# Kernel tuning notes

Measured on AMD Instinct MI355X. Metric: run time of the kernel, lower is better.

The kernel has to match this reference:

```python
import jax, jax.numpy as jnp
import numpy as np

INPUT_SIZE = 512
HIDDEN_SIZE = 512
BATCH = 16384


def _layer_norm(x, gamma, beta, eps=1e-5):
    mean = jnp.mean(x, axis=-1, keepdims=True)
    var = jnp.var(x, axis=-1, keepdims=True)
    return (x - mean) * jax.lax.rsqrt(var + eps) * gamma + beta


def setup_inputs() -> dict:
    key = jax.random.key(0)
    ks = jax.random.split(key, 4)
    H = HIDDEN_SIZE
    x = jax.random.normal(ks[0], (BATCH, INPUT_SIZE), dtype=jnp.float32)
    h = jax.random.normal(ks[1], (BATCH, H), dtype=jnp.float32)
    # Linear weights stored torch-style as [out_features, in_features]
    W_i2h = jax.random.normal(ks[2], (3 * H, INPUT_SIZE), dtype=jnp.float32) / np.sqrt(INPUT_SIZE)
    W_h2h = jax.random.normal(ks[3], (3 * H, H), dtype=jnp.float32) / np.sqrt(H)
    return {
        "x": x,
        "h": h,
        "W_i2h": W_i2h,
        "W_h2h": W_h2h,
        "g_r": jnp.ones((H,), jnp.float32), "b_r": jnp.zeros((H,), jnp.float32),
        "g_z": jnp.ones((H,), jnp.float32), "b_z": jnp.zeros((H,), jnp.float32),
        "g_n": jnp.ones((H,), jnp.float32), "b_n": jnp.zeros((H,), jnp.float32),
    }


def reference(x, h, W_i2h, W_h2h, g_r, b_r, g_z, b_z, g_n, b_n):
    H = h.shape[-1]
    x_gates = x @ W_i2h.T  # [B, 3H]
    h_gates = h @ W_h2h.T  # [B, 3H]
    x_r, x_z, x_n = jnp.split(x_gates, 3, axis=1)
    h_r, h_z, h_n = jnp.split(h_gates, 3, axis=1)
    r = jax.nn.sigmoid(_layer_norm(x_r + h_r, g_r, b_r))
    z = jax.nn.sigmoid(_layer_norm(x_z + h_z, g_z, b_z))
    n = jnp.tanh(_layer_norm(x_n + r * h_n, g_n, b_n))
    h_new = (1.0 - z) * n + z * h
    return h_new
```

## Files before the change

### kernel.cpp

```cpp
#include <hip/hip_runtime.h>

#define BATCH 16384
#define BM    64
#define NT    1024

typedef float f32x4 __attribute__((ext_vector_type(4)));
typedef short s16x8 __attribute__((ext_vector_type(8)));

__device__ __forceinline__ unsigned short f2bf(float f) {
  unsigned u = __float_as_uint(f);
  u = (u + 0x7fffu + ((u >> 16) & 1u)) >> 16;
  return (unsigned short)u;
}
__device__ __forceinline__ float bflo(unsigned p) { return __uint_as_float(p << 16); }
__device__ __forceinline__ float bfhi(unsigned p) { return __uint_as_float(p & 0xffff0000u); }

__global__ __launch_bounds__(256) void wconv_kernel(
    const float* __restrict__ wx, const float* __restrict__ wh,
    unsigned short* __restrict__ dst) {
  int i = blockIdx.x * 256 + threadIdx.x;
  const float4* src = (i < 196608) ? (const float4*)wx
                                   : ((const float4*)wh) - 196608;
  float4 v = src[i];
  ushort4 p = {f2bf(v.x), f2bf(v.y), f2bf(v.z), f2bf(v.w)};
  ((ushort4*)dst)[i] = p;
}

__global__ __launch_bounds__(NT, 4) void gru_fused_kernel(
    const float* __restrict__ x, const float* __restrict__ h,
    const unsigned short* __restrict__ Wxb, const unsigned short* __restrict__ Whb,
    const float* __restrict__ g_r, const float* __restrict__ b_r,
    const float* __restrict__ g_z, const float* __restrict__ b_z,
    const float* __restrict__ g_n, const float* __restrict__ b_n,
    float* __restrict__ out) {
  __shared__ __align__(16) unsigned short At[2][BM * 512];
  __shared__ float red[BM][33];
  __shared__ float rstat[BM][2];

  const int tid  = threadIdx.x;
  const int lane = tid & 63;
  const int w    = tid >> 6;
  const int l15  = lane & 15;
  const int lg   = lane >> 4;
  const int rowbase = blockIdx.x * BM;
  const int c0 = w * 32 + l15, c1 = c0 + 16;

  {
    const float4* x4 = (const float4*)x;
    const float4* h4 = (const float4*)h;
    const int sr = tid >> 7, sc4 = tid & 127;
#pragma unroll
    for (int p = 0; p < 8; ++p) {
      int r = p * 8 + sr;
      float4 vx = x4[(size_t)(rowbase + r) * 128 + sc4];
      float4 vh = h4[(size_t)(rowbase + r) * 128 + sc4];
      int bo = (r * 1024 + sc4 * 8) ^ ((r & 7) << 4);
      ushort4 px = {f2bf(vx.x), f2bf(vx.y), f2bf(vx.z), f2bf(vx.w)};
      ushort4 ph = {f2bf(vh.x), f2bf(vh.y), f2bf(vh.z), f2bf(vh.w)};
      *(ushort4*)((char*)At[0] + bo) = px;
      *(ushort4*)((char*)At[1] + bo) = ph;
    }
  }
  __syncthreads();

  f32x4 acc[4][2];

#define ZERO_ACC                                                               \
  _Pragma("unroll")                                                            \
  for (int rf = 0; rf < 4; ++rf)                                               \
    _Pragma("unroll")                                                          \
    for (int cf = 0; cf < 2; ++cf) acc[rf][cf] = (f32x4){0.f, 0.f, 0.f, 0.f};

#define KLOOP(ATP, WPTR, GBASE)                                                \
  {                                                                            \
    const char* wbase = (const char*)(WPTR);                                   \
    _Pragma("unroll 2")                                                        \
    for (int kk = 0; kk < 16; ++kk) {                                          \
      s16x8 af[4];                                                             \
      _Pragma("unroll")                                                        \
      for (int rf = 0; rf < 4; ++rf) {                                         \
        int row = rf * 16 + l15;                                               \
        int bo = (row * 1024 + kk * 64 + lg * 16) ^ ((row & 7) << 4);          \
        af[rf] = *(const s16x8*)((const char*)(ATP) + bo);                     \
      }                                                                        \
      s16x8 bf[2];                                                             \
      _Pragma("unroll")                                                        \
      for (int cf = 0; cf < 2; ++cf) {                                         \
        int wrow = (GBASE) + w * 32 + cf * 16 + l15;                           \
        bf[cf] = *(const s16x8*)(wbase + ((size_t)wrow * 512 + lg * 8) * 2 + kk * 64); \
      }                                                                        \
      _Pragma("unroll")                                                        \
      for (int rf = 0; rf < 4; ++rf)                                           \
        _Pragma("unroll")                                                      \
        for (int cf = 0; cf < 2; ++cf)                                         \
          acc[rf][cf] = __builtin_amdgcn_mfma_f32_16x16x32_bf16(af[rf], bf[cf], acc[rf][cf], 0, 0, 0); \
    }                                                                          \
  }

#define REDUCE_STATS                                                           \
  {                                                                            \
    _Pragma("unroll")                                                          \
    for (int rf = 0; rf < 4; ++rf) {                                           \
      _Pragma("unroll")                                                        \
      for (int rg = 0; rg < 4; ++rg) {                                         \
        float v0 = acc[rf][0][rg], v1 = acc[rf][1][rg];                        \
        float s = v0 + v1, q = v0 * v0 + v1 * v1;                              \
        s += __shfl_xor(s, 1); q += __shfl_xor(q, 1);                          \
        s += __shfl_xor(s, 2); q += __shfl_xor(q, 2);                          \
        s += __shfl_xor(s, 4); q += __shfl_xor(q, 4);                          \
        s += __shfl_xor(s, 8); q += __shfl_xor(q, 8);                          \
        if (l15 == 0) {                                                        \
          red[rf * 16 + lg * 4 + rg][w * 2]     = s;                           \
          red[rf * 16 + lg * 4 + rg][w * 2 + 1] = q;                           \
        }                                                                      \
      }                                                                        \
    }                                                                          \
    __syncthreads();                                                           \
    if (tid < 64) {                                                            \
      float s = 0.f, q = 0.f;                                                  \
      _Pragma("unroll")                                                        \
      for (int ww = 0; ww < 16; ++ww) {                                        \
        s += red[tid][ww * 2];                                                 \
        q += red[tid][ww * 2 + 1];                                             \
      }                                                                        \
      float mean = s * (1.0f / 512.0f);                                        \
      float var  = q * (1.0f / 512.0f) - mean * mean;                          \
      rstat[tid][0] = mean;                                                    \
      rstat[tid][1] = rsqrtf(var + 1e-5f);                                     \
    }                                                                          \
    __syncthreads();                                                           \
  }

  ZERO_ACC
  KLOOP(At[0], Wxb, 0)
  KLOOP(At[1], Whb, 0)
  REDUCE_STATS

  unsigned rp[4][2][2];
  {
    float ga[2] = {g_r[c0], g_r[c1]}, be[2] = {b_r[c0], b_r[c1]};
#pragma unroll
    for (int rf = 0; rf < 4; ++rf)
#pragma unroll
      for (int rg = 0; rg < 4; rg += 2) {
        int row0 = rf * 16 + lg * 4 + rg;
        float m0 = rstat[row0][0], s0 = rstat[row0][1];
        float m1 = rstat[row0 + 1][0], s1 = rstat[row0 + 1][1];
#pragma unroll
        for (int cf = 0; cf < 2; ++cf) {
          float r0 = (acc[rf][cf][rg] - m0) * s0 * ga[cf] + be[cf];
          float r1 = (acc[rf][cf][rg + 1] - m1) * s1 * ga[cf] + be[cf];
          r0 = 1.0f / (1.0f + __expf(-r0));
          r1 = 1.0f / (1.0f + __expf(-r1));
          rp[rf][cf][rg >> 1] = (unsigned)f2bf(r0) | ((unsigned)f2bf(r1) << 16);
        }
      }
  }

  ZERO_ACC
  KLOOP(At[1], Whb, 1024)
#pragma unroll
  for (int rf = 0; rf < 4; ++rf)
#pragma unroll
    for (int cf = 0; cf < 2; ++cf) {
      acc[rf][cf][0] *= bflo(rp[rf][cf][0]);
      acc[rf][cf][1] *= bfhi(rp[rf][cf][0]);
      acc[rf][cf][2] *= bflo(rp[rf][cf][1]);
      acc[rf][cf][3] *= bfhi(rp[rf][cf][1]);
    }
  KLOOP(At[0], Wxb, 1024)
  REDUCE_STATS

  f32x4 nv[4][2];
  {
    float ga[2] = {g_n[c0], g_n[c1]}, be[2] = {b_n[c0], b_n[c1]};
#pragma unroll
    for (int rf = 0; rf < 4; ++rf)
#pragma unroll
      for (int rg = 0; rg < 4; ++rg) {
        int row = rf * 16 + lg * 4 + rg;
        float m = rstat[row][0], sd = rstat[row][1];
#pragma unroll
        for (int cf = 0; cf < 2; ++cf) {
          float arg = (acc[rf][cf][rg] - m) * sd * ga[cf] + be[cf];
          arg = fminf(fmaxf(arg, -20.f), 20.f);
          float e = __expf(2.0f * arg);
          nv[rf][cf][rg] = (e - 1.0f) / (e + 1.0f);
        }
      }
  }

  ZERO_ACC
  KLOOP(At[0], Wxb, 512)
  KLOOP(At[1], Whb, 512)
  REDUCE_STATS

  {
    float ga[2] = {g_z[c0], g_z[c1]}, be[2] = {b_z[c0], b_z[c1]};
#pragma unroll
    for (int rf = 0; rf < 4; ++rf)
#pragma unroll
      for (int rg = 0; rg < 4; ++rg) {
        int row = rf * 16 + lg * 4 + rg;
        float m = rstat[row][0], sd = rstat[row][1];
        int grow = rowbase + row;
#pragma unroll
        for (int cf = 0; cf < 2; ++cf) {
          float zv = (acc[rf][cf][rg] - m) * sd * ga[cf] + be[cf];
          zv = 1.0f / (1.0f + __expf(-zv));
          int gcol = w * 32 + cf * 16 + l15;
          float hval = h[(size_t)grow * 512 + gcol];
          float n = nv[rf][cf][rg];
          out[(size_t)grow * 512 + gcol] = n + zv * (hval - n);
        }
      }
  }
}

extern "C" void kernel_launch(void* const* d_in, const int* in_sizes, int n_in,
                              void* d_out, int out_size, void* d_ws, size_t ws_size,
                              hipStream_t stream) {
  const float* x  = (const float*)d_in[0];
  const float* h  = (const float*)d_in[1];
  const float* wx = (const float*)d_in[2];
  const float* wh = (const float*)d_in[3];
  const float* g_r = (const float*)d_in[4];
  const float* b_r = (const float*)d_in[5];
  const float* g_z = (const float*)d_in[6];
  const float* b_z = (const float*)d_in[7];
  const float* g_n = (const float*)d_in[8];
  const float* b_n = (const float*)d_in[9];
  float* out = (float*)d_out;

  unsigned short* wbf = (unsigned short*)d_ws;

  wconv_kernel<<<1536, 256, 0, stream>>>(wx, wh, wbf);
  gru_fused_kernel<<<BATCH / BM, NT, 0, stream>>>(
      x, h, wbf, wbf + 1536 * 512, g_r, b_r, g_z, b_z, g_n, b_n, out);
}
```

Baseline: 233.6 us.

## Split batch across a 512-thread register-pipelined kernel and the original kernel

Adds a new 512-thread kernel where each wave computes 64 columns with 4x4 accumulator fragments and double-buffered A/B register prefetch across the K loop. It handles the first 160 row blocks, and the original 1024-thread kernel handles the remaining 96 blocks, launched as a second kernel with a row offset. The aim is more MFMA work per loaded fragment and better hiding of weight-load latency, plus an uneven split that fits one wave of blocks on the CUs. The cost is higher register pressure (waves_per_eu 2) and a second serialized launch on the same stream, which may leave tail imbalance.

```diff
diff --git a/kernel.cpp b/kernel.cpp
--- a/kernel.cpp
+++ b/kernel.cpp
@@ -2,7 +2,9 @@
 
 #define BATCH 16384
 #define BM    64
-#define NT    1024
+#define NT    512
+#define NA_BLOCKS 160
+#define NB_BLOCKS 96
 
 typedef float f32x4 __attribute__((ext_vector_type(4)));
 typedef short s16x8 __attribute__((ext_vector_type(8)));
@@ -26,7 +28,9 @@
   ((ushort4*)dst)[i] = p;
 }
 
-__global__ __launch_bounds__(NT, 4) void gru_fused_kernel(
+__global__
+__attribute__((amdgpu_flat_work_group_size(NT, NT), amdgpu_waves_per_eu(2, 2)))
+void gru_pipe_kernel(
     const float* __restrict__ x, const float* __restrict__ h,
     const unsigned short* __restrict__ Wxb, const unsigned short* __restrict__ Whb,
     const float* __restrict__ g_r, const float* __restrict__ b_r,
@@ -34,7 +38,7 @@
     const float* __restrict__ g_n, const float* __restrict__ b_n,
     float* __restrict__ out) {
   __shared__ __align__(16) unsigned short At[2][BM * 512];
-  __shared__ float red[BM][33];
+  __shared__ float red[BM][17];
   __shared__ float rstat[BM][2];
 
   const int tid  = threadIdx.x;
@@ -43,6 +47,218 @@
   const int l15  = lane & 15;
   const int lg   = lane >> 4;
   const int rowbase = blockIdx.x * BM;
+  const int cb = w * 64 + l15;
+
+  {
+    const float4* x4 = (const float4*)x;
+    const float4* h4 = (const float4*)h;
+    const int sr = tid >> 7, sc4 = tid & 127;
+#pragma unroll
+    for (int p = 0; p < 16; ++p) {
+      int r = p * 4 + sr;
+      float4 vx = x4[(size_t)(rowbase + r) * 128 + sc4];
+      float4 vh = h4[(size_t)(rowbase + r) * 128 + sc4];
+      int bo = (r * 1024 + sc4 * 8) ^ ((r & 7) << 4);
+      ushort4 px = {f2bf(vx.x), f2bf(vx.y), f2bf(vx.z), f2bf(vx.w)};
+      ushort4 ph = {f2bf(vh.x), f2bf(vh.y), f2bf(vh.z), f2bf(vh.w)};
+      *(ushort4*)((char*)At[0] + bo) = px;
+      *(ushort4*)((char*)At[1] + bo) = ph;
+    }
+  }
+  __syncthreads();
+
+  f32x4 acc[4][4];
+
+#define ZERO_ACC                                                               \
+  _Pragma("unroll")                                                            \
+  for (int rf = 0; rf < 4; ++rf)                                               \
+    _Pragma("unroll")                                                          \
+    for (int cf = 0; cf < 4; ++cf) acc[rf][cf] = (f32x4){0.f, 0.f, 0.f, 0.f};
+
+#define LOADA(DST, ATP, KK)                                                    \
+  {                                                                            \
+    _Pragma("unroll")                                                          \
+    for (int rf = 0; rf < 4; ++rf) {                                           \
+      int row = rf * 16 + l15;                                                 \
+      int bo = (row * 1024 + (KK) * 64 + lg * 16) ^ ((row & 7) << 4);          \
+      (DST)[rf] = *(const s16x8*)((const char*)(ATP) + bo);                    \
+    }                                                                          \
+  }
+
+#define KLOOP(ATP, WPTR, GBASE)                                                \
+  {                                                                            \
+    const char* wbp[4];                                                        \
+    _Pragma("unroll")                                                          \
+    for (int cf = 0; cf < 4; ++cf)                                             \
+      wbp[cf] = (const char*)(WPTR) +                                          \
+          ((size_t)((GBASE) + w * 64 + cf * 16 + l15) * 512 + lg * 8) * 2;     \
+    s16x8 af[2][4];                                                            \
+    s16x8 bq[2][4];                                                            \
+    LOADA(af[0], ATP, 0)                                                       \
+    _Pragma("unroll")                                                          \
+    for (int cf = 0; cf < 4; ++cf) bq[0][cf] = *(const s16x8*)(wbp[cf]);       \
+    _Pragma("unroll")                                                          \
+    for (int kk = 0; kk < 16; ++kk) {                                          \
+      if (kk < 15) {                                                           \
+        LOADA(af[(kk + 1) & 1], ATP, kk + 1)                                   \
+        _Pragma("unroll")                                                      \
+        for (int cf = 0; cf < 4; ++cf)                                         \
+          bq[(kk + 1) & 1][cf] = *(const s16x8*)(wbp[cf] + (kk + 1) * 64);     \
+      }                                                                        \
+      _Pragma("unroll")                                                        \
+      for (int rf = 0; rf < 4; ++rf)                                           \
+        _Pragma("unroll")                                                      \
+        for (int cf = 0; cf < 4; ++cf)                                         \
+          acc[rf][cf] = __builtin_amdgcn_mfma_f32_16x16x32_bf16(               \
+              af[kk & 1][rf], bq[kk & 1][cf], acc[rf][cf], 0, 0, 0);           \
+    }                                                                          \
+  }
+
+#define REDUCE_STATS                                                           \
+  {                                                                            \
+    _Pragma("unroll")                                                          \
+    for (int rf = 0; rf < 4; ++rf) {                                           \
+      _Pragma("unroll")                                                        \
+      for (int rg = 0; rg < 4; ++rg) {                                         \
+        float v0 = acc[rf][0][rg], v1 = acc[rf][1][rg];                        \
+        float v2 = acc[rf][2][rg], v3 = acc[rf][3][rg];                        \
+        float s = (v0 + v1) + (v2 + v3);                                       \
+        float q = (v0 * v0 + v1 * v1) + (v2 * v2 + v3 * v3);                   \
+        s += __shfl_xor(s, 1); q += __shfl_xor(q, 1);                          \
+        s += __shfl_xor(s, 2); q += __shfl_xor(q, 2);                          \
+        s += __shfl_xor(s, 4); q += __shfl_xor(q, 4);                          \
+        s += __shfl_xor(s, 8); q += __shfl_xor(q, 8);                          \
+        if (l15 == 0) {                                                        \
+          red[rf * 16 + lg * 4 + rg][w * 2]     = s;                           \
+          red[rf * 16 + lg * 4 + rg][w * 2 + 1] = q;                           \
+        }                                                                      \
+      }                                                                        \
+    }                                                                          \
+    __syncthreads();                                                           \
+    if (tid < 64) {                                                            \
+      float s = 0.f, q = 0.f;                                                  \
+      _Pragma("unroll")                                                        \
+      for (int ww = 0; ww < 8; ++ww) {                                         \
+        s += red[tid][ww * 2];                                                 \
+        q += red[tid][ww * 2 + 1];                                             \
+      }                                                                        \
+      float mean = s * (1.0f / 512.0f);                                        \
+      float var  = q * (1.0f / 512.0f) - mean * mean;                          \
+      rstat[tid][0] = mean;                                                    \
+      rstat[tid][1] = rsqrtf(var + 1e-5f);                                     \
+    }                                                                          \
+    __syncthreads();                                                           \
+  }
+
+  ZERO_ACC
+  KLOOP(At[0], Wxb, 0)
+  KLOOP(At[1], Whb, 0)
+  REDUCE_STATS
+
+  unsigned rp[4][4][2];
+  {
+    float ga[4], be[4];
+#pragma unroll
+    for (int cf = 0; cf < 4; ++cf) { ga[cf] = g_r[cb + cf * 16]; be[cf] = b_r[cb + cf * 16]; }
+#pragma unroll
+    for (int rf = 0; rf < 4; ++rf)
+#pragma unroll
+      for (int rg = 0; rg < 4; rg += 2) {
+        int row0 = rf * 16 + lg * 4 + rg;
+        float m0 = rstat[row0][0], s0 = rstat[row0][1];
+        float m1 = rstat[row0 + 1][0], s1 = rstat[row0 + 1][1];
+#pragma unroll
+        for (int cf = 0; cf < 4; ++cf) {
+          float r0 = (acc[rf][cf][rg] - m0) * s0 * ga[cf] + be[cf];
+          float r1 = (acc[rf][cf][rg + 1] - m1) * s1 * ga[cf] + be[cf];
+          r0 = 1.0f / (1.0f + __expf(-r0));
+          r1 = 1.0f / (1.0f + __expf(-r1));
+          rp[rf][cf][rg >> 1] = (unsigned)f2bf(r0) | ((unsigned)f2bf(r1) << 16);
+        }
+      }
+  }
+
+  ZERO_ACC
+  KLOOP(At[1], Whb, 1024)
+#pragma unroll
+  for (int rf = 0; rf < 4; ++rf)
+#pragma unroll
+    for (int cf = 0; cf < 4; ++cf) {
+      acc[rf][cf][0] *= bflo(rp[rf][cf][0]);
+      acc[rf][cf][1] *= bfhi(rp[rf][cf][0]);
+      acc[rf][cf][2] *= bflo(rp[rf][cf][1]);
+      acc[rf][cf][3] *= bfhi(rp[rf][cf][1]);
+    }
+  KLOOP(At[0], Wxb, 1024)
+  REDUCE_STATS
+
+  f32x4 nv[4][4];
+  {
+    float ga[4], be[4];
+#pragma unroll
+    for (int cf = 0; cf < 4; ++cf) { ga[cf] = g_n[cb + cf * 16]; be[cf] = b_n[cb + cf * 16]; }
+#pragma unroll
+    for (int rf = 0; rf < 4; ++rf)
+#pragma unroll
+      for (int rg = 0; rg < 4; ++rg) {
+        int row = rf * 16 + lg * 4 + rg;
+        float m = rstat[row][0], sd = rstat[row][1];
+#pragma unroll
+        for (int cf = 0; cf < 4; ++cf) {
+          float arg = (acc[rf][cf][rg] - m) * sd * ga[cf] + be[cf];
+          arg = fminf(fmaxf(arg, -20.f), 20.f);
+          float e = __expf(2.0f * arg);
+          nv[rf][cf][rg] = (e - 1.0f) / (e + 1.0f);
+        }
+      }
+  }
+
+  ZERO_ACC
+  KLOOP(At[0], Wxb, 512)
+  KLOOP(At[1], Whb, 512)
+  REDUCE_STATS
+
+  {
+    float ga[4], be[4];
+#pragma unroll
+    for (int cf = 0; cf < 4; ++cf) { ga[cf] = g_z[cb + cf * 16]; be[cf] = b_z[cb + cf * 16]; }
+#pragma unroll
+    for (int rf = 0; rf < 4; ++rf)
+#pragma unroll
+      for (int rg = 0; rg < 4; ++rg) {
+        int row = rf * 16 + lg * 4 + rg;
+        float m = rstat[row][0], sd = rstat[row][1];
+        int grow = rowbase + row;
+#pragma unroll
+        for (int cf = 0; cf < 4; ++cf) {
+          float zv = (acc[rf][cf][rg] - m) * sd * ga[cf] + be[cf];
+          zv = 1.0f / (1.0f + __expf(-zv));
+          int gcol = w * 64 + cf * 16 + l15;
+          float hval = h[(size_t)grow * 512 + gcol];
+          float n = nv[rf][cf][rg];
+          out[(size_t)grow * 512 + gcol] = n + zv * (hval - n);
+        }
+      }
+  }
+}
+
+__global__ __launch_bounds__(1024, 4) void gru_base_kernel(
+    const float* __restrict__ x, const float* __restrict__ h,
+    const unsigned short* __restrict__ Wxb, const unsigned short* __restrict__ Whb,
+    const float* __restrict__ g_r, const float* __restrict__ b_r,
+    const float* __restrict__ g_z, const float* __restrict__ b_z,
+    const float* __restrict__ g_n, const float* __restrict__ b_n,
+    float* __restrict__ out, int rowoff) {
+  __shared__ __align__(16) unsigned short At[2][BM * 512];
+  __shared__ float red[BM][33];
+  __shared__ float rstat[BM][2];
+
+  const int tid  = threadIdx.x;
+  const int lane = tid & 63;
+  const int w    = tid >> 6;
+  const int l15  = lane & 15;
+  const int lg   = lane >> 4;
+  const int rowbase = rowoff + blockIdx.x * BM;
   const int c0 = w * 32 + l15, c1 = c0 + 16;
 
   {
@@ -65,13 +281,13 @@
 
   f32x4 acc[4][2];
 
-#define ZERO_ACC                                                               \
+#define ZERO_ACC_B                                                             \
   _Pragma("unroll")                                                            \
   for (int rf = 0; rf < 4; ++rf)                                               \
     _Pragma("unroll")                                                          \
     for (int cf = 0; cf < 2; ++cf) acc[rf][cf] = (f32x4){0.f, 0.f, 0.f, 0.f};
 
-#define KLOOP(ATP, WPTR, GBASE)                                                \
+#define KLOOP_B(ATP, WPTR, GBASE)                                              \
   {                                                                            \
     const char* wbase = (const char*)(WPTR);                                   \
     _Pragma("unroll 2")                                                        \
@@ -97,7 +313,7 @@
     }                                                                          \
   }
 
-#define REDUCE_STATS                                                           \
+#define REDUCE_STATS_B                                                         \
   {                                                                            \
     _Pragma("unroll")                                                          \
     for (int rf = 0; rf < 4; ++rf) {                                           \
@@ -131,10 +347,10 @@
     __syncthreads();                                                           \
   }
 
-  ZERO_ACC
-  KLOOP(At[0], Wxb, 0)
-  KLOOP(At[1], Whb, 0)
-  REDUCE_STATS
+  ZERO_ACC_B
+  KLOOP_B(At[0], Wxb, 0)
+  KLOOP_B(At[1], Whb, 0)
+  REDUCE_STATS_B
 
   unsigned rp[4][2][2];
   {
@@ -157,8 +373,8 @@
       }
   }
 
-  ZERO_ACC
-  KLOOP(At[1], Whb, 1024)
+  ZERO_ACC_B
+  KLOOP_B(At[1], Whb, 1024)
 #pragma unroll
   for (int rf = 0; rf < 4; ++rf)
 #pragma unroll
@@ -168,8 +384,8 @@
       acc[rf][cf][2] *= bflo(rp[rf][cf][1]);
       acc[rf][cf][3] *= bfhi(rp[rf][cf][1]);
     }
-  KLOOP(At[0], Wxb, 1024)
-  REDUCE_STATS
+  KLOOP_B(At[0], Wxb, 1024)
+  REDUCE_STATS_B
 
   f32x4 nv[4][2];
   {
@@ -190,10 +406,10 @@
       }
   }
 
-  ZERO_ACC
-  KLOOP(At[0], Wxb, 512)
-  KLOOP(At[1], Whb, 512)
-  REDUCE_STATS
+  ZERO_ACC_B
+  KLOOP_B(At[0], Wxb, 512)
+  KLOOP_B(At[1], Whb, 512)
+  REDUCE_STATS_B
 
   {
     float ga[2] = {g_z[c0], g_z[c1]}, be[2] = {b_z[c0], b_z[c1]};
@@ -235,6 +451,9 @@
   unsigned short* wbf = (unsigned short*)d_ws;
 
   wconv_kernel<<<1536, 256, 0, stream>>>(wx, wh, wbf);
-  gru_fused_kernel<<<BATCH / BM, NT, 0, stream>>>(
+  gru_pipe_kernel<<<NA_BLOCKS, NT, 0, stream>>>(
       x, h, wbf, wbf + 1536 * 512, g_r, b_r, g_z, b_z, g_n, b_n, out);
+  gru_base_kernel<<<NB_BLOCKS, 1024, 0, stream>>>(
+      x, h, wbf, wbf + 1536 * 512, g_r, b_r, g_z, b_z, g_n, b_n, out,
+      NA_BLOCKS * BM);
 }
```

Measured after the change: 350.2 us. 49.9% more time.
